# Kernel tuning notes

Hardware: AMD Instinct MI355X
Metric: run time of the kernel (lower is better)

Reference implementation:

```python
import jax, jax.numpy as jnp
import numpy as np
from jax import lax

# Lens/aperture geometry (must match init_kwargs lens_mask)
LENS = 21
RADIUS = LENS // 2
EPS = 1e-8


def _offsets():
    """Flattened 21x21 aperture footprint: distance kernel, circular lens mask,
    and (row, col) slice offsets into the padded image."""
    ys, xs = np.meshgrid(np.arange(LENS), np.arange(LENS), indexing='ij')
    dy = ys - RADIUS
    dx = xs - RADIUS
    dist = np.sqrt(dy * dy + dx * dx).astype(np.float32)
    mask = (dist <= RADIUS).astype(np.float32)
    return (jnp.asarray(dist.ravel()), jnp.asarray(mask.ravel()),
            jnp.asarray(ys.ravel().astype(np.int32)),
            jnp.asarray(xs.ravel().astype(np.int32)))


def scatter_layer(x5, lens_effect):
    """Scatter (splat) defocus rendering of one RGBAD layer.

    x5: [B,5,H,W] (r,g,b,alpha,relative-disparity); lens_effect: [B,1].
    Each source pixel splats its premultiplied color over a disk of radius
    r = |disp| * lens_effect (soft-edged, area-normalized). Because the disk
    kernel is symmetric in the offset, the scatter is computed as a gather
    over the 21x21 footprint with weights taken from the *source* pixel.

    Returns [B,5,H,W]: [:3] accumulated rgb, [3] accumulated weight,
    [4] occupancy (clipped accumulated alpha-weight).
    """
    B, _, H, W = x5.shape
    dist, mask, oy, ox = _offsets()
    rgb, a, disp = x5[:, :3], x5[:, 3:4], x5[:, 4:5]
    r = jnp.clip(jnp.abs(disp) * lens_effect[:, :, None, None], 0.0, float(RADIUS))  # [B,1,H,W]

    # per-source-pixel soft disk area: sum_o mask(o) * clip(r + 0.5 - dist(o), 0, 1)
    def area_step(acc, dm):
        d, m = dm
        return acc + m * jnp.clip(r + 0.5 - d, 0.0, 1.0), None

    area, _ = lax.scan(area_step, jnp.zeros_like(r), (dist, mask))

    # premultiplied source energy, normalized by splat area
    s = jnp.concatenate([rgb * a, a], axis=1) / (area + EPS)  # [B,4,H,W]
    pad = ((0, 0), (0, 0), (RADIUS, RADIUS), (RADIUS, RADIUS))
    s_pad = jnp.pad(s, pad)
    r_pad = jnp.pad(r, pad)

    # gather formulation of the scatter: out[q] = sum_o s[q-o] * w(o; r[q-o])
    def step(acc, dmyx):
        d, m, dy, dx = dmyx
        sl = lax.dynamic_slice(s_pad, (0, 0, dy, dx), (B, 4, H, W))
        rsl = lax.dynamic_slice(r_pad, (0, 0, dy, dx), (B, 1, H, W))
        w = m * jnp.clip(rsl + 0.5 - d, 0.0, 1.0)
        return acc + sl * w, None

    out4, _ = lax.scan(step, jnp.zeros((B, 4, H, W), x5.dtype), (dist, mask, oy, ox))
    occu = jnp.clip(out4[:, 3:4], 0.0, 1.0)
    return jnp.concatenate([out4, occu], axis=1)


def setup_inputs() -> dict:
    key = jax.random.key(0)
    k1, k2 = jax.random.split(key)
    B, N_LAYER, H, W = 2, 3, 512, 512
    rgbad_layers = jax.random.uniform(k1, (B, 5 * N_LAYER, H, W), dtype=jnp.float32)
    # lens strength in a range that exercises the full 21x21 footprint
    lens_effect = jax.random.uniform(k2, (B, 1), dtype=jnp.float32) * 10.0
    focal = jnp.zeros((B, 5 * N_LAYER, H, W), dtype=jnp.float32)
    return {"rgbad_layers": rgbad_layers, "lens_effect": lens_effect, "focal": focal}


def reference(rgbad_layers, lens_effect, focal):
    """Multi_Layer_Renderer.forward: front-to-back alpha compositing of
    per-layer scatter-rendered bokeh."""
    x = rgbad_layers - focal
    n_layer = x.shape[1] // 5
    blurs = [scatter_layer(x[:, 5 * i:5 * (i + 1)], lens_effect) for i in range(n_layer)]
    rgb0, w0, o0 = blurs[0][:, :3], blurs[0][:, 3:4], blurs[0][:, 4:5]
    blur_rgb = rgb0 / (w0 + EPS) * o0
    trans = 1.0 - o0  # accumulated transmittance
    for li in range(1, n_layer):
        lr, lw, lo = blurs[li][:, :3], blurs[li][:, 3:4], blurs[li][:, 4:5]
        blur_rgb = blur_rgb + lr / (lw + EPS) * (trans * lo)
        trans = trans * (1.0 - lo)
    return blur_rgb
```

## Files before the change

### kernel.cpp

```cpp
#include <hip/hip_runtime.h>
#include <hip/hip_bf16.h>

#define HH 512
#define WW 512
#define HWSZ (512*512)

typedef _Float16 hh4 __attribute__((ext_vector_type(4)));
typedef _Float16 hh2 __attribute__((ext_vector_type(2)));
typedef float    ff4 __attribute__((ext_vector_type(4)));

__device__ __forceinline__ float clamp01(float x) {
    return __builtin_amdgcn_fmed3f(x, 0.0f, 1.0f);
}
__device__ __forceinline__ hh2 clamp01h2(hh2 x) {
    const hh2 z = {(_Float16)0.0f, (_Float16)0.0f};
    const hh2 o = {(_Float16)1.0f, (_Float16)1.0f};
    return __builtin_elementwise_min(__builtin_elementwise_max(x, z), o);
}
__device__ __forceinline__ hh2 pkrtz(float a, float b) {
    return __builtin_bit_cast(hh2, __builtin_amdgcn_cvt_pkrtz(a, b));
}

__global__ __launch_bounds__(256, 2)
void mlr_fused_kernel(const float* __restrict__ rgbad,
                      const float* __restrict__ lens_eff,
                      const float* __restrict__ focal,
                      float* __restrict__ out,
                      int nbx, int B)
{
    constexpr int TW = 64, TH = 16;
    constexpr int SW = 88;
    constexpr int SH = TH + 20;
    constexpr int LP = 90;
    constexpr int NG = SW / 4;
    constexpr int NSLOT = SH * NG;
    constexpr int NIT = (NSLOT + 255) / 256;

    __shared__ uint2 sP[SH * LP];
    __shared__ uint  rP[SH * LP / 2];
    __shared__ int   maxbits;

    const int tx  = threadIdx.x;
    const int ty  = threadIdx.y;
    const int tid = ty * 16 + tx;
    const int bid = blockIdx.x;
    const int bb  = bid % B;
    const int t   = bid / B;
    const int bx0 = (t % nbx) * TW;
    const int by0 = (t / nbx) * TH;
    const float lens = lens_eff[bb];

    static constexpr float DJ[44] = {
        0.f, 1.f, 1.41421356f, 2.f, 2.23606798f, 2.82842712f, 3.f, 3.16227766f,
        3.60555128f, 4.f, 4.12310563f, 4.24264069f, 4.47213595f, 5.f, 5.09901951f,
        5.38516481f, 5.65685425f, 5.83095189f, 6.f, 6.08276253f, 6.32455532f,
        6.40312424f, 6.70820393f, 7.f, 7.07106781f, 7.21110255f, 7.28010989f,
        7.61577311f, 7.81024968f, 8.f, 8.06225775f, 8.24621125f, 8.48528137f,
        8.54400375f, 8.60232527f, 8.94427191f, 9.f, 9.05538514f, 9.21954446f,
        9.43398113f, 9.48683298f, 9.84885780f, 9.89949494f, 10.f };
    static constexpr float CNT[44] = {
        1,4,4,4,8,4,4,8,8,4,8,4,8,12,8,8,4,8,4,8,8,8,
        8,4,12,8,8,8,8,4,16,8,4,8,8,8,4,8,16,8,8,8,4,12 };

    float blurR[4] = {0,0,0,0}, blurG[4] = {0,0,0,0}, blurB[4] = {0,0,0,0};
    float trans[4] = {1,1,1,1};

#pragma unroll 1
    for (int l = 0; l < 3; ++l) {
        __syncthreads();
        if (tid == 0) maxbits = 0;
        __syncthreads();

        const float* pin = rgbad + (size_t)(bb * 15 + 5 * l) * HWSZ;
        const float* pfo = focal + (size_t)(bb * 15 + 5 * l) * HWSZ;
        float mloc = 0.f;

#pragma unroll
        for (int it = 0; it < NIT; ++it) {
            int s = tid + it * 256;
            s = (s < NSLOT) ? s : (NSLOT - 1);
            const int row = s / NG;
            const int grp = s - row * NG;
            const int gy  = by0 - 10 + row;
            const int gx0 = bx0 - 12 + 4 * grp;

            ff4 i0 = {0,0,0,0}, i1 = {0,0,0,0}, i2 = {0,0,0,0}, i3 = {0,0,0,0}, i4 = {0,0,0,0};
            ff4 f0 = {0,0,0,0}, f1 = {0,0,0,0}, f2 = {0,0,0,0}, f3 = {0,0,0,0}, f4 = {0,0,0,0};
            const bool valid = ((unsigned)gy < (unsigned)HH) && ((unsigned)gx0 < (unsigned)WW);
            if (valid) {
                const size_t off = (size_t)gy * WW + (size_t)gx0;
                i0 = *reinterpret_cast<const ff4*>(pin + off);
                i1 = *reinterpret_cast<const ff4*>(pin + off +   HWSZ);
                i2 = *reinterpret_cast<const ff4*>(pin + off + 2*HWSZ);
                i3 = *reinterpret_cast<const ff4*>(pin + off + 3*HWSZ);
                i4 = *reinterpret_cast<const ff4*>(pin + off + 4*HWSZ);
                f0 = *reinterpret_cast<const ff4*>(pfo + off);
                f1 = *reinterpret_cast<const ff4*>(pfo + off +   HWSZ);
                f2 = *reinterpret_cast<const ff4*>(pfo + off + 2*HWSZ);
                f3 = *reinterpret_cast<const ff4*>(pfo + off + 3*HWSZ);
                f4 = *reinterpret_cast<const ff4*>(pfo + off + 4*HWSZ);
            }
            uint2 pk[4];
            unsigned short rh[4];
#pragma unroll
            for (int k = 0; k < 4; ++k) {
                const float cr = i0[k] - f0[k];
                const float cg = i1[k] - f1[k];
                const float cb = i2[k] - f2[k];
                const float ca = i3[k] - f3[k];
                const float cd = i4[k] - f4[k];
                const float r  = fminf(fabsf(cd) * lens, 10.f);
                const float rp05 = r + 0.5f;
                const hh2 rp2s = pkrtz(rp05, rp05);
                float aacc = 0.f;
#pragma unroll
                for (int j = 0; j < 44; j += 2) {
                    const hh2 dj2 = {(_Float16)DJ[j], (_Float16)DJ[j + 1]};
                    const hh2 c2  = {(_Float16)CNT[j], (_Float16)CNT[j + 1]};
                    const hh2 w2  = clamp01h2(rp2s - dj2);
                    aacc = __builtin_amdgcn_fdot2(w2, c2, aacc, false);
                }
                const float inv = 1.0f / (aacc + 1e-8f);
                const float pa  = ca * inv;
                hh4 hv;
                hv.x = (_Float16)(cr * pa);
                hv.y = (_Float16)(cg * pa);
                hv.z = (_Float16)(cb * pa);
                hv.w = (_Float16)pa;
                pk[k] = __builtin_bit_cast(uint2, hv);
                rh[k] = __builtin_bit_cast(unsigned short, (_Float16)rp05);
                mloc  = fmaxf(mloc, rp05);
            }
            const int base = row * LP + 4 * grp;
            uint4 s01, s23;
            s01.x = pk[0].x; s01.y = pk[0].y; s01.z = pk[1].x; s01.w = pk[1].y;
            s23.x = pk[2].x; s23.y = pk[2].y; s23.z = pk[3].x; s23.w = pk[3].y;
            *reinterpret_cast<uint4*>(&sP[base])     = s01;
            *reinterpret_cast<uint4*>(&sP[base + 2]) = s23;
            uint2 rr2;
            rr2.x = (uint)rh[0] | ((uint)rh[1] << 16);
            rr2.y = (uint)rh[2] | ((uint)rh[3] << 16);
            *reinterpret_cast<uint2*>(&rP[base >> 1]) = rr2;
        }
        atomicMax(&maxbits, __float_as_int(mloc));
        __syncthreads();

        const float rmax = __int_as_float(maxbits);
        const int U = min(10, (int)ceilf(rmax) - 1);

        float accR[4] = {0,0,0,0}, accG[4] = {0,0,0,0};
        float accB[4] = {0,0,0,0}, accW[4] = {0,0,0,0};

#define PCOMP(SP, RPW, v0) { \
            const hh2 rp2 = __builtin_bit_cast(hh2, (RPW)); \
            const hh2 cR = __builtin_bit_cast(hh2, __builtin_amdgcn_perm((SP).z, (SP).x, 0x05040100u)); \
            const hh2 cG = __builtin_bit_cast(hh2, __builtin_amdgcn_perm((SP).z, (SP).x, 0x07060302u)); \
            const hh2 cB = __builtin_bit_cast(hh2, __builtin_amdgcn_perm((SP).w, (SP).y, 0x05040100u)); \
            const hh2 cA = __builtin_bit_cast(hh2, __builtin_amdgcn_perm((SP).w, (SP).y, 0x07060302u)); \
            _Pragma("unroll") \
            for (int ox = 0; ox < 4; ++ox) { \
                const hh2 w2 = clamp01h2(rp2 - hdd2[(v0) - ox + 13]); \
                accR[ox] = __builtin_amdgcn_fdot2(cR, w2, accR[ox], false); \
                accG[ox] = __builtin_amdgcn_fdot2(cG, w2, accG[ox], false); \
                accB[ox] = __builtin_amdgcn_fdot2(cB, w2, accB[ox], false); \
                accW[ox] = __builtin_amdgcn_fdot2(cA, w2, accW[ox], false); \
            } }

#define DLOAD(nm, v0) \
            const uint4 spA_##nm = *reinterpret_cast<const uint4*>(&sP[rbA + (v0)]); \
            const uint  rpA_##nm = rP[(rbA + (v0)) >> 1]; \
            const uint4 spB_##nm = *reinterpret_cast<const uint4*>(&sP[rbB + (v0)]); \
            const uint  rpB_##nm = rP[(rbB + (v0)) >> 1];
#define DCOMP(nm, v0) PCOMP(spA_##nm, rpA_##nm, v0) PCOMP(spB_##nm, rpB_##nm, v0)
#define SLOAD(nm, v0) \
            const uint4 spA_##nm = *reinterpret_cast<const uint4*>(&sP[rbA + (v0)]); \
            const uint  rpA_##nm = rP[(rbA + (v0)) >> 1];
#define SCOMP(nm, v0) PCOMP(spA_##nm, rpA_##nm, v0)

        {
            hh2 hdd2[26];
#pragma unroll
            for (int m = 0; m < 26; ++m) {
                const int dxa = m - 13, dxb = dxa + 1;
                const float qa = (float)(dxa * dxa);
                const float qb = (float)(dxb * dxb);
                const float da = (qa <= 100.0f) ? __builtin_sqrtf(qa) : 3000.0f;
                const float db = (qb <= 100.0f) ? __builtin_sqrtf(qb) : 3000.0f;
                hdd2[m] = pkrtz(da, db);
            }
            const float vm2 = rmax * rmax;
            const int rbA = (ty + 10) * LP + 12 + 4 * tx;
            SLOAD(c0, -2) SLOAD(c1, 0) SLOAD(c2, 2) SLOAD(c3, 4)
            SCOMP(c0, -2) SCOMP(c1, 0) SCOMP(c2, 2) SCOMP(c3, 4)
            if (vm2 > 9.0f) {
                SLOAD(d0, -6) SLOAD(d1, -4) SLOAD(d2, 6) SLOAD(d3, 8)
                SCOMP(d0, -6) SCOMP(d1, -4) SCOMP(d2, 6) SCOMP(d3, 8)
            }
            if (vm2 > 36.0f) {
                SLOAD(e0, -8) SLOAD(e1, 10)
                SCOMP(e0, -8) SCOMP(e1, 10)
            }
            if (vm2 > 81.0f) {
                SLOAD(f0, -10) SLOAD(f1, 12)
                SCOMP(f0, -10) SCOMP(f1, 12)
            }
        }

#pragma unroll 1
        for (int au = 1; au <= U; ++au) {
            const float u2f = (float)(au * au);
            const float vm2 = rmax * rmax - u2f;
            hh2 hdd2[26];
#pragma unroll
            for (int m = 0; m < 26; ++m) {
                const int dxa = m - 13, dxb = dxa + 1;
                const float qa = u2f + (float)(dxa * dxa);
                const float qb = u2f + (float)(dxb * dxb);
                const float da = (qa <= 100.0f) ? __builtin_sqrtf(qa) : 3000.0f;
                const float db = (qb <= 100.0f) ? __builtin_sqrtf(qb) : 3000.0f;
                hdd2[m] = pkrtz(da, db);
            }
            const int rbA = (ty + 10 + au) * LP + 12 + 4 * tx;
            const int rbB = (ty + 10 - au) * LP + 12 + 4 * tx;

            DLOAD(c0, -2) DLOAD(c1, 0) DLOAD(c2, 2) DLOAD(c3, 4)
            DCOMP(c0, -2) DCOMP(c1, 0) DCOMP(c2, 2) DCOMP(c3, 4)
            if (vm2 > 9.0f) {
                DLOAD(d0, -6) DLOAD(d1, -4) DLOAD(d2, 6) DLOAD(d3, 8)
                DCOMP(d0, -6) DCOMP(d1, -4) DCOMP(d2, 6) DCOMP(d3, 8)
            }
            if (vm2 > 36.0f) {
                DLOAD(e0, -8) DLOAD(e1, 10)
                DCOMP(e0, -8) DCOMP(e1, 10)
            }
            if (vm2 > 81.0f) {
                DLOAD(f0, -10) DLOAD(f1, 12)
                DCOMP(f0, -10) DCOMP(f1, 12)
            }
        }
#undef PCOMP
#undef DLOAD
#undef DCOMP
#undef SLOAD
#undef SCOMP

#pragma unroll
        for (int ox = 0; ox < 4; ++ox) {
            const float wsum = accW[ox];
            const float occ  = clamp01(wsum);
            const float f    = trans[ox] * occ / (wsum + 1e-8f);
            blurR[ox] = fmaf(accR[ox], f, blurR[ox]);
            blurG[ox] = fmaf(accG[ox], f, blurG[ox]);
            blurB[ox] = fmaf(accB[ox], f, blurB[ox]);
            trans[ox] *= (1.0f - occ);
        }
    }

    const int oy = by0 + ty;
    const size_t obase = (size_t)bb * 3 * HWSZ + (size_t)oy * WW + (size_t)(bx0 + 4 * tx);

    float4 vR, vG, vB;
    vR.x = blurR[0]; vR.y = blurR[1]; vR.z = blurR[2]; vR.w = blurR[3];
    vG.x = blurG[0]; vG.y = blurG[1]; vG.z = blurG[2]; vG.w = blurG[3];
    vB.x = blurB[0]; vB.y = blurB[1]; vB.z = blurB[2]; vB.w = blurB[3];

    *reinterpret_cast<float4*>(out + obase)            = vR;
    *reinterpret_cast<float4*>(out + obase + HWSZ)     = vG;
    *reinterpret_cast<float4*>(out + obase + 2 * HWSZ) = vB;
}

extern "C" void kernel_launch(void* const* d_in, const int* in_sizes, int n_in,
                              void* d_out, int out_size, void* d_ws, size_t ws_size,
                              hipStream_t stream) {
    const float* rgbad = (const float*)d_in[0];
    const float* lens  = (const float*)d_in[1];
    const float* focal = (const float*)d_in[2];
    float* out = (float*)d_out;
    const int B = in_sizes[1];
    const int nbx = WW / 64;
    const int nby = HH / 16;
    dim3 grid(nbx * nby * B, 1, 1);
    dim3 block(16, 16, 1);
    hipLaunchKernelGGL(mlr_fused_kernel, grid, block, 0, stream,
                       rgbad, lens, focal, out, nbx, B);
}
```

Before: 42.86 us.

## Double-buffer LDS staging and prefetch next layer's global loads during compute

Splits the staging into issue/commit helpers and double-buffers the shared-memory tiles so the next layer's global loads are issued before the current layer's gather and committed afterwards. This removes two barriers per layer and hides global-load latency behind the stencil work. It also reorganises the LDS reads to fetch packed radius values as 64-bit pairs shared between neighbouring taps, nests the radius-threshold branches, and changes the LDS row pitch from 90 to 92. In exchange it doubles shared-memory use and keeps 40 prefetched float4s live in registers, which may raise pressure or lower occupancy.

New measurement: 42.02 us, median of 2. No clear change (-2.0%).

```diff
diff --git a/kernel.cpp b/kernel.cpp
--- a/kernel.cpp
+++ b/kernel.cpp
@@ -8,6 +8,13 @@
 typedef _Float16 hh4 __attribute__((ext_vector_type(4)));
 typedef _Float16 hh2 __attribute__((ext_vector_type(2)));
 typedef float    ff4 __attribute__((ext_vector_type(4)));
+
+constexpr int TW = 64, TH = 16;
+constexpr int SW = 88;
+constexpr int SH = TH + 20;
+constexpr int LP = 92;
+constexpr int NG = SW / 4;
+constexpr int NSLOT = SH * NG;
 
 __device__ __forceinline__ float clamp01(float x) {
     return __builtin_amdgcn_fmed3f(x, 0.0f, 1.0f);
@@ -21,35 +28,40 @@
     return __builtin_bit_cast(hh2, __builtin_amdgcn_cvt_pkrtz(a, b));
 }
 
-__global__ __launch_bounds__(256, 2)
-void mlr_fused_kernel(const float* __restrict__ rgbad,
-                      const float* __restrict__ lens_eff,
-                      const float* __restrict__ focal,
-                      float* __restrict__ out,
-                      int nbx, int B)
-{
-    constexpr int TW = 64, TH = 16;
-    constexpr int SW = 88;
-    constexpr int SH = TH + 20;
-    constexpr int LP = 90;
-    constexpr int NG = SW / 4;
-    constexpr int NSLOT = SH * NG;
-    constexpr int NIT = (NSLOT + 255) / 256;
-
-    __shared__ uint2 sP[SH * LP];
-    __shared__ uint  rP[SH * LP / 2];
-    __shared__ int   maxbits;
-
-    const int tx  = threadIdx.x;
-    const int ty  = threadIdx.y;
-    const int tid = ty * 16 + tx;
-    const int bid = blockIdx.x;
-    const int bb  = bid % B;
-    const int t   = bid / B;
-    const int bx0 = (t % nbx) * TW;
-    const int by0 = (t / nbx) * TH;
-    const float lens = lens_eff[bb];
-
+struct StageRegs { ff4 v[2][10]; };
+
+__device__ __forceinline__ StageRegs stage_issue(const float* __restrict__ pin,
+                                                 const float* __restrict__ pfo,
+                                                 int tid, int bx0, int by0, int itBase) {
+    StageRegs R;
+#pragma unroll
+    for (int k = 0; k < 2; ++k) {
+        int s = tid + (itBase + k) * 256;
+        s = (s < NSLOT) ? s : (NSLOT - 1);
+        const int row = s / NG;
+        const int grp = s - row * NG;
+        const int gy  = by0 - 10 + row;
+        const int gx0 = bx0 - 12 + 4 * grp;
+        const ff4 z = {0, 0, 0, 0};
+#pragma unroll
+        for (int c = 0; c < 10; ++c) R.v[k][c] = z;
+        if (((unsigned)gy < (unsigned)HH) && ((unsigned)gx0 < (unsigned)WW)) {
+            const size_t off = (size_t)gy * WW + (size_t)gx0;
+#pragma unroll
+            for (int c = 0; c < 5; ++c)
+                R.v[k][c] = *reinterpret_cast<const ff4*>(pin + off + (size_t)c * HWSZ);
+#pragma unroll
+            for (int c = 0; c < 5; ++c)
+                R.v[k][5 + c] = *reinterpret_cast<const ff4*>(pfo + off + (size_t)c * HWSZ);
+        }
+    }
+    return R;
+}
+
+__device__ __forceinline__ void stage_commit(const StageRegs& R, float lens,
+                                             int tid, int itBase,
+                                             uint2* __restrict__ sPb, uint* __restrict__ rPb,
+                                             float& mloc) {
     static constexpr float DJ[44] = {
         0.f, 1.f, 1.41421356f, 2.f, 2.23606798f, 2.82842712f, 3.f, 3.16227766f,
         3.60555128f, 4.f, 4.12310563f, 4.24264069f, 4.47213595f, 5.f, 5.09901951f,
@@ -62,101 +74,118 @@
         1,4,4,4,8,4,4,8,8,4,8,4,8,12,8,8,4,8,4,8,8,8,
         8,4,12,8,8,8,8,4,16,8,4,8,8,8,4,8,16,8,8,8,4,12 };
 
+#pragma unroll
+    for (int k = 0; k < 2; ++k) {
+        int s = tid + (itBase + k) * 256;
+        s = (s < NSLOT) ? s : (NSLOT - 1);
+        const int row = s / NG;
+        const int grp = s - row * NG;
+        uint2 pk[4];
+        unsigned short rh[4];
+#pragma unroll
+        for (int j = 0; j < 4; ++j) {
+            const float cr = R.v[k][0][j] - R.v[k][5][j];
+            const float cg = R.v[k][1][j] - R.v[k][6][j];
+            const float cb = R.v[k][2][j] - R.v[k][7][j];
+            const float ca = R.v[k][3][j] - R.v[k][8][j];
+            const float cd = R.v[k][4][j] - R.v[k][9][j];
+            const float r  = fminf(fabsf(cd) * lens, 10.f);
+            const float rp05 = r + 0.5f;
+            const hh2 rp2s = pkrtz(rp05, rp05);
+            float aacc = 0.f;
+#pragma unroll
+            for (int j2 = 0; j2 < 44; j2 += 2) {
+                const hh2 dj2 = {(_Float16)DJ[j2], (_Float16)DJ[j2 + 1]};
+                const hh2 c2  = {(_Float16)CNT[j2], (_Float16)CNT[j2 + 1]};
+                const hh2 w2  = clamp01h2(rp2s - dj2);
+                aacc = __builtin_amdgcn_fdot2(w2, c2, aacc, false);
+            }
+            const float inv = 1.0f / (aacc + 1e-8f);
+            const float pa  = ca * inv;
+            hh4 hv;
+            hv.x = (_Float16)(cr * pa);
+            hv.y = (_Float16)(cg * pa);
+            hv.z = (_Float16)(cb * pa);
+            hv.w = (_Float16)pa;
+            pk[j] = __builtin_bit_cast(uint2, hv);
+            rh[j] = __builtin_bit_cast(unsigned short, (_Float16)rp05);
+            mloc  = fmaxf(mloc, rp05);
+        }
+        const int base = row * LP + 4 * grp;
+        uint4 s01, s23;
+        s01.x = pk[0].x; s01.y = pk[0].y; s01.z = pk[1].x; s01.w = pk[1].y;
+        s23.x = pk[2].x; s23.y = pk[2].y; s23.z = pk[3].x; s23.w = pk[3].y;
+        *reinterpret_cast<uint4*>(&sPb[base])     = s01;
+        *reinterpret_cast<uint4*>(&sPb[base + 2]) = s23;
+        uint2 rr2;
+        rr2.x = (uint)rh[0] | ((uint)rh[1] << 16);
+        rr2.y = (uint)rh[2] | ((uint)rh[3] << 16);
+        *reinterpret_cast<uint2*>(&rPb[base >> 1]) = rr2;
+    }
+}
+
+__global__ __launch_bounds__(256, 2)
+void mlr_fused_kernel(const float* __restrict__ rgbad,
+                      const float* __restrict__ lens_eff,
+                      const float* __restrict__ focal,
+                      float* __restrict__ out,
+                      int nbx, int B)
+{
+    __shared__ uint2 sP[2][SH * LP];
+    __shared__ uint  rP[2][SH * LP / 2];
+    __shared__ int   mb[3];
+
+    const int tx  = threadIdx.x;
+    const int ty  = threadIdx.y;
+    const int tid = ty * 16 + tx;
+    const int bid = blockIdx.x;
+    const int bb  = bid % B;
+    const int t   = bid / B;
+    const int bx0 = (t % nbx) * TW;
+    const int by0 = (t / nbx) * TH;
+    const float lens = lens_eff[bb];
+
+    if (tid < 3) mb[tid] = 0;
+    __syncthreads();
+
     float blurR[4] = {0,0,0,0}, blurG[4] = {0,0,0,0}, blurB[4] = {0,0,0,0};
     float trans[4] = {1,1,1,1};
 
+    {
+        const float* pin = rgbad + (size_t)(bb * 15) * HWSZ;
+        const float* pfo = focal + (size_t)(bb * 15) * HWSZ;
+        StageRegs a = stage_issue(pin, pfo, tid, bx0, by0, 0);
+        StageRegs b = stage_issue(pin, pfo, tid, bx0, by0, 2);
+        float mloc = 0.f;
+        stage_commit(a, lens, tid, 0, sP[0], rP[0], mloc);
+        stage_commit(b, lens, tid, 2, sP[0], rP[0], mloc);
+        atomicMax(&mb[0], __float_as_int(mloc));
+    }
+    __syncthreads();
+
 #pragma unroll 1
     for (int l = 0; l < 3; ++l) {
-        __syncthreads();
-        if (tid == 0) maxbits = 0;
-        __syncthreads();
-
-        const float* pin = rgbad + (size_t)(bb * 15 + 5 * l) * HWSZ;
-        const float* pfo = focal + (size_t)(bb * 15 + 5 * l) * HWSZ;
-        float mloc = 0.f;
-
-#pragma unroll
-        for (int it = 0; it < NIT; ++it) {
-            int s = tid + it * 256;
-            s = (s < NSLOT) ? s : (NSLOT - 1);
-            const int row = s / NG;
-            const int grp = s - row * NG;
-            const int gy  = by0 - 10 + row;
-            const int gx0 = bx0 - 12 + 4 * grp;
-
-            ff4 i0 = {0,0,0,0}, i1 = {0,0,0,0}, i2 = {0,0,0,0}, i3 = {0,0,0,0}, i4 = {0,0,0,0};
-            ff4 f0 = {0,0,0,0}, f1 = {0,0,0,0}, f2 = {0,0,0,0}, f3 = {0,0,0,0}, f4 = {0,0,0,0};
-            const bool valid = ((unsigned)gy < (unsigned)HH) && ((unsigned)gx0 < (unsigned)WW);
-            if (valid) {
-                const size_t off = (size_t)gy * WW + (size_t)gx0;
-                i0 = *reinterpret_cast<const ff4*>(pin + off);
-                i1 = *reinterpret_cast<const ff4*>(pin + off +   HWSZ);
-                i2 = *reinterpret_cast<const ff4*>(pin + off + 2*HWSZ);
-                i3 = *reinterpret_cast<const ff4*>(pin + off + 3*HWSZ);
-                i4 = *reinterpret_cast<const ff4*>(pin + off + 4*HWSZ);
-                f0 = *reinterpret_cast<const ff4*>(pfo + off);
-                f1 = *reinterpret_cast<const ff4*>(pfo + off +   HWSZ);
-                f2 = *reinterpret_cast<const ff4*>(pfo + off + 2*HWSZ);
-                f3 = *reinterpret_cast<const ff4*>(pfo + off + 3*HWSZ);
-                f4 = *reinterpret_cast<const ff4*>(pfo + off + 4*HWSZ);
-            }
-            uint2 pk[4];
-            unsigned short rh[4];
-#pragma unroll
-            for (int k = 0; k < 4; ++k) {
-                const float cr = i0[k] - f0[k];
-                const float cg = i1[k] - f1[k];
-                const float cb = i2[k] - f2[k];
-                const float ca = i3[k] - f3[k];
-                const float cd = i4[k] - f4[k];
-                const float r  = fminf(fabsf(cd) * lens, 10.f);
-                const float rp05 = r + 0.5f;
-                const hh2 rp2s = pkrtz(rp05, rp05);
-                float aacc = 0.f;
-#pragma unroll
-                for (int j = 0; j < 44; j += 2) {
-                    const hh2 dj2 = {(_Float16)DJ[j], (_Float16)DJ[j + 1]};
-                    const hh2 c2  = {(_Float16)CNT[j], (_Float16)CNT[j + 1]};
-                    const hh2 w2  = clamp01h2(rp2s - dj2);
-                    aacc = __builtin_amdgcn_fdot2(w2, c2, aacc, false);
-                }
-                const float inv = 1.0f / (aacc + 1e-8f);
-                const float pa  = ca * inv;
-                hh4 hv;
-                hv.x = (_Float16)(cr * pa);
-                hv.y = (_Float16)(cg * pa);
-                hv.z = (_Float16)(cb * pa);
-                hv.w = (_Float16)pa;
-                pk[k] = __builtin_bit_cast(uint2, hv);
-                rh[k] = __builtin_bit_cast(unsigned short, (_Float16)rp05);
-                mloc  = fmaxf(mloc, rp05);
-            }
-            const int base = row * LP + 4 * grp;
-            uint4 s01, s23;
-            s01.x = pk[0].x; s01.y = pk[0].y; s01.z = pk[1].x; s01.w = pk[1].y;
-            s23.x = pk[2].x; s23.y = pk[2].y; s23.z = pk[3].x; s23.w = pk[3].y;
-            *reinterpret_cast<uint4*>(&sP[base])     = s01;
-            *reinterpret_cast<uint4*>(&sP[base + 2]) = s23;
-            uint2 rr2;
-            rr2.x = (uint)rh[0] | ((uint)rh[1] << 16);
-            rr2.y = (uint)rh[2] | ((uint)rh[3] << 16);
-            *reinterpret_cast<uint2*>(&rP[base >> 1]) = rr2;
-        }
-        atomicMax(&maxbits, __float_as_int(mloc));
-        __syncthreads();
-
-        const float rmax = __int_as_float(maxbits);
+        const int cur = l & 1;
+        const float rmax = __int_as_float(mb[l]);
         const int U = min(10, (int)ceilf(rmax) - 1);
+
+        uint2* const sPc = sP[cur];
+        uint*  const rPc = rP[cur];
+
+        const float* pinN = rgbad + (size_t)(bb * 15 + 5 * (l + 1)) * HWSZ;
+        const float* pfoN = focal + (size_t)(bb * 15 + 5 * (l + 1)) * HWSZ;
+        StageRegs pre;
+        if (l < 2) pre = stage_issue(pinN, pfoN, tid, bx0, by0, 0);
 
         float accR[4] = {0,0,0,0}, accG[4] = {0,0,0,0};
         float accB[4] = {0,0,0,0}, accW[4] = {0,0,0,0};
 
-#define PCOMP(SP, RPW, v0) { \
-            const hh2 rp2 = __builtin_bit_cast(hh2, (RPW)); \
-            const hh2 cR = __builtin_bit_cast(hh2, __builtin_amdgcn_perm((SP).z, (SP).x, 0x05040100u)); \
-            const hh2 cG = __builtin_bit_cast(hh2, __builtin_amdgcn_perm((SP).z, (SP).x, 0x07060302u)); \
-            const hh2 cB = __builtin_bit_cast(hh2, __builtin_amdgcn_perm((SP).w, (SP).y, 0x05040100u)); \
-            const hh2 cA = __builtin_bit_cast(hh2, __builtin_amdgcn_perm((SP).w, (SP).y, 0x07060302u)); \
+#define PCOMP(SP_, RPH_, v0) { \
+            const hh2 rp2 = __builtin_bit_cast(hh2, (RPH_)); \
+            const hh2 cR = __builtin_bit_cast(hh2, __builtin_amdgcn_perm((SP_).z, (SP_).x, 0x05040100u)); \
+            const hh2 cG = __builtin_bit_cast(hh2, __builtin_amdgcn_perm((SP_).z, (SP_).x, 0x07060302u)); \
+            const hh2 cB = __builtin_bit_cast(hh2, __builtin_amdgcn_perm((SP_).w, (SP_).y, 0x05040100u)); \
+            const hh2 cA = __builtin_bit_cast(hh2, __builtin_amdgcn_perm((SP_).w, (SP_).y, 0x07060302u)); \
             _Pragma("unroll") \
             for (int ox = 0; ox < 4; ++ox) { \
                 const hh2 w2 = clamp01h2(rp2 - hdd2[(v0) - ox + 13]); \
@@ -165,17 +194,8 @@
                 accB[ox] = __builtin_amdgcn_fdot2(cB, w2, accB[ox], false); \
                 accW[ox] = __builtin_amdgcn_fdot2(cA, w2, accW[ox], false); \
             } }
-
-#define DLOAD(nm, v0) \
-            const uint4 spA_##nm = *reinterpret_cast<const uint4*>(&sP[rbA + (v0)]); \
-            const uint  rpA_##nm = rP[(rbA + (v0)) >> 1]; \
-            const uint4 spB_##nm = *reinterpret_cast<const uint4*>(&sP[rbB + (v0)]); \
-            const uint  rpB_##nm = rP[(rbB + (v0)) >> 1];
-#define DCOMP(nm, v0) PCOMP(spA_##nm, rpA_##nm, v0) PCOMP(spB_##nm, rpB_##nm, v0)
-#define SLOAD(nm, v0) \
-            const uint4 spA_##nm = *reinterpret_cast<const uint4*>(&sP[rbA + (v0)]); \
-            const uint  rpA_##nm = rP[(rbA + (v0)) >> 1];
-#define SCOMP(nm, v0) PCOMP(spA_##nm, rpA_##nm, v0)
+#define LDQ(nm, rb, off)  const uint2 nm = *reinterpret_cast<const uint2*>(&rPc[((rb) + (off)) >> 1]);
+#define LD128(nm, rb, off) const uint4 nm = *reinterpret_cast<const uint4*>(&sPc[(rb) + (off)]);
 
         {
             hh2 hdd2[26];
@@ -190,19 +210,22 @@
             }
             const float vm2 = rmax * rmax;
             const int rbA = (ty + 10) * LP + 12 + 4 * tx;
-            SLOAD(c0, -2) SLOAD(c1, 0) SLOAD(c2, 2) SLOAD(c3, 4)
-            SCOMP(c0, -2) SCOMP(c1, 0) SCOMP(c2, 2) SCOMP(c3, 4)
+            LDQ(qAm4, rbA, -4) LDQ(qA0, rbA, 0) LDQ(qA4, rbA, 4)
+            LD128(sAm2, rbA, -2) LD128(sA0, rbA, 0) LD128(sA2, rbA, 2) LD128(sA4, rbA, 4)
+            PCOMP(sAm2, qAm4.y, -2) PCOMP(sA0, qA0.x, 0) PCOMP(sA2, qA0.y, 2) PCOMP(sA4, qA4.x, 4)
             if (vm2 > 9.0f) {
-                SLOAD(d0, -6) SLOAD(d1, -4) SLOAD(d2, 6) SLOAD(d3, 8)
-                SCOMP(d0, -6) SCOMP(d1, -4) SCOMP(d2, 6) SCOMP(d3, 8)
-            }
-            if (vm2 > 36.0f) {
-                SLOAD(e0, -8) SLOAD(e1, 10)
-                SCOMP(e0, -8) SCOMP(e1, 10)
-            }
-            if (vm2 > 81.0f) {
-                SLOAD(f0, -10) SLOAD(f1, 12)
-                SCOMP(f0, -10) SCOMP(f1, 12)
+                LDQ(qAm8, rbA, -8) LDQ(qA8, rbA, 8)
+                LD128(sAm6, rbA, -6) LD128(sAm4, rbA, -4) LD128(sA6, rbA, 6) LD128(sA8, rbA, 8)
+                PCOMP(sAm6, qAm8.y, -6) PCOMP(sAm4, qAm4.x, -4) PCOMP(sA6, qA4.y, 6) PCOMP(sA8, qA8.x, 8)
+                if (vm2 > 36.0f) {
+                    LD128(sAm8, rbA, -8) LD128(sA10, rbA, 10)
+                    PCOMP(sAm8, qAm8.x, -8) PCOMP(sA10, qA8.y, 10)
+                    if (vm2 > 81.0f) {
+                        LDQ(qAm12, rbA, -12) LDQ(qA12, rbA, 12)
+                        LD128(sAm10, rbA, -10) LD128(sA12, rbA, 12)
+                        PCOMP(sAm10, qAm12.y, -10) PCOMP(sA12, qA12.x, 12)
+                    }
+                }
             }
         }
 
@@ -223,26 +246,46 @@
             const int rbA = (ty + 10 + au) * LP + 12 + 4 * tx;
             const int rbB = (ty + 10 - au) * LP + 12 + 4 * tx;
 
-            DLOAD(c0, -2) DLOAD(c1, 0) DLOAD(c2, 2) DLOAD(c3, 4)
-            DCOMP(c0, -2) DCOMP(c1, 0) DCOMP(c2, 2) DCOMP(c3, 4)
+            LDQ(qAm4, rbA, -4) LDQ(qA0, rbA, 0) LDQ(qA4, rbA, 4)
+            LD128(sAm2, rbA, -2) LD128(sA0, rbA, 0) LD128(sA2, rbA, 2) LD128(sA4, rbA, 4)
+            LDQ(qBm4, rbB, -4) LDQ(qB0, rbB, 0) LDQ(qB4, rbB, 4)
+            LD128(sBm2, rbB, -2) LD128(sB0, rbB, 0) LD128(sB2, rbB, 2) LD128(sB4, rbB, 4)
+            PCOMP(sAm2, qAm4.y, -2) PCOMP(sA0, qA0.x, 0) PCOMP(sA2, qA0.y, 2) PCOMP(sA4, qA4.x, 4)
+            PCOMP(sBm2, qBm4.y, -2) PCOMP(sB0, qB0.x, 0) PCOMP(sB2, qB0.y, 2) PCOMP(sB4, qB4.x, 4)
             if (vm2 > 9.0f) {
-                DLOAD(d0, -6) DLOAD(d1, -4) DLOAD(d2, 6) DLOAD(d3, 8)
-                DCOMP(d0, -6) DCOMP(d1, -4) DCOMP(d2, 6) DCOMP(d3, 8)
-            }
-            if (vm2 > 36.0f) {
-                DLOAD(e0, -8) DLOAD(e1, 10)
-                DCOMP(e0, -8) DCOMP(e1, 10)
-            }
-            if (vm2 > 81.0f) {
-                DLOAD(f0, -10) DLOAD(f1, 12)
-                DCOMP(f0, -10) DCOMP(f1, 12)
+                LDQ(qAm8, rbA, -8) LDQ(qA8, rbA, 8)
+                LD128(sAm6, rbA, -6) LD128(sAm4, rbA, -4) LD128(sA6, rbA, 6) LD128(sA8, rbA, 8)
+                LDQ(qBm8, rbB, -8) LDQ(qB8, rbB, 8)
+                LD128(sBm6, rbB, -6) LD128(sBm4, rbB, -4) LD128(sB6, rbB, 6) LD128(sB8, rbB, 8)
+                PCOMP(sAm6, qAm8.y, -6) PCOMP(sAm4, qAm4.x, -4) PCOMP(sA6, qA4.y, 6) PCOMP(sA8, qA8.x, 8)
+                PCOMP(sBm6, qBm8.y, -6) PCOMP(sBm4, qBm4.x, -4) PCOMP(sB6, qB4.y, 6) PCOMP(sB8, qB8.x, 8)
+                if (vm2 > 36.0f) {
+                    LD128(sAm8, rbA, -8) LD128(sA10, rbA, 10)
+                    LD128(sBm8, rbB, -8) LD128(sB10, rbB, 10)
+                    PCOMP(sAm8, qAm8.x, -8) PCOMP(sA10, qA8.y, 10)
+                    PCOMP(sBm8, qBm8.x, -8) PCOMP(sB10, qB8.y, 10)
+                    if (vm2 > 81.0f) {
+                        LDQ(qAm12, rbA, -12) LDQ(qA12, rbA, 12)
+                        LD128(sAm10, rbA, -10) LD128(sA12, rbA, 12)
+                        LDQ(qBm12, rbB, -12) LDQ(qB12, rbB, 12)
+                        LD128(sBm10, rbB, -10) LD128(sB12, rbB, 12)
+                        PCOMP(sAm10, qAm12.y, -10) PCOMP(sA12, qA12.x, 12)
+                        PCOMP(sBm10, qBm12.y, -10) PCOMP(sB12, qB12.x, 12)
+                    }
+                }
             }
         }
 #undef PCOMP
-#undef DLOAD
-#undef DCOMP
-#undef SLOAD
-#undef SCOMP
+#undef LDQ
+#undef LD128
+
+        if (l < 2) {
+            StageRegs pre2 = stage_issue(pinN, pfoN, tid, bx0, by0, 2);
+            float mloc = 0.f;
+            stage_commit(pre,  lens, tid, 0, sP[cur ^ 1], rP[cur ^ 1], mloc);
+            stage_commit(pre2, lens, tid, 2, sP[cur ^ 1], rP[cur ^ 1], mloc);
+            atomicMax(&mb[l + 1], __float_as_int(mloc));
+        }
 
 #pragma unroll
         for (int ox = 0; ox < 4; ++ox) {
@@ -254,6 +297,7 @@
             blurB[ox] = fmaf(accB[ox], f, blurB[ox]);
             trans[ox] *= (1.0f - occ);
         }
+        __syncthreads();
     }
 
     const int oy = by0 + ty;
```
